# Performance work log

Hardware: AMD Instinct MI355X
Metric: run time of the kernel (lower is better)

Reference implementation:

```python
import jax, jax.numpy as jnp
import numpy as np

B, S, D, H, E, FF = 8, 512, 768, 12, 8, 3072
HD = D // H

def layernorm(x, g, b, eps=1e-5):
    mu = jnp.mean(x, axis=-1, keepdims=True)
    var = jnp.mean((x - mu) ** 2, axis=-1, keepdims=True)
    return (x - mu) * jax.lax.rsqrt(var + eps) * g + b

def setup_inputs() -> dict:
    key = jax.random.key(0)
    ks = jax.random.split(key, 16)
    sd = lambda n: 1.0 / np.sqrt(n)
    return {
        "x": jax.random.normal(ks[0], (B, S, D), jnp.float32),
        "indexes_list": jax.random.randint(ks[1], (1,), 0, E),
        "ln1_g": jnp.ones((D,), jnp.float32),
        "ln1_b": jnp.zeros((D,), jnp.float32),
        "qkv_w": jax.random.normal(ks[2], (D, 3 * D), jnp.float32) * sd(D),
        "proj_w": jax.random.normal(ks[3], (D, D), jnp.float32) * sd(D),
        "proj_b": jnp.zeros((D,), jnp.float32),
        "ln2_g": jnp.ones((D,), jnp.float32),
        "ln2_b": jnp.zeros((D,), jnp.float32),
        "switch_w": jax.random.normal(ks[4], (D, E), jnp.float32) * sd(D),
        "switch_b": jnp.zeros((E,), jnp.float32),
        "w1": jax.random.normal(ks[5], (E, D, FF), jnp.float32) * sd(D),
        "b1": jnp.zeros((E, FF), jnp.float32),
        "w2": jax.random.normal(ks[6], (E, FF, D), jnp.float32) * sd(FF),
        "b2": jnp.zeros((E, D), jnp.float32),
    }

def reference(x, indexes_list, ln1_g, ln1_b, qkv_w, proj_w, proj_b,
              ln2_g, ln2_b, switch_w, switch_b, w1, b1, w2, b2):
    # --- attention sublayer ---
    h = layernorm(x, ln1_g, ln1_b)
    qkv = (h @ qkv_w).reshape(B, S, 3, H, HD).transpose(2, 0, 3, 1, 4)  # [3,B,H,S,hd]
    q, k, v = qkv[0], qkv[1], qkv[2]
    scale = HD ** -0.5
    attn = jax.nn.softmax(jnp.einsum('bhqd,bhkd->bhqk', q, k) * scale, axis=-1)
    o = jnp.einsum('bhqk,bhkd->bhqd', attn, v).transpose(0, 2, 1, 3).reshape(B, S, D)
    x = x + o @ proj_w + proj_b
    # --- switch MoE sublayer (routes arg ignored, as in original) ---
    h = layernorm(x, ln2_g, ln2_b).reshape(B * S, D)  # [T,D]
    logits = h @ switch_w + switch_b
    routes = jnp.argmax(jax.nn.softmax(logits, axis=-1), axis=-1)  # [T]
    # dense per-expert compute, then select by route (same math as gather/scatter)
    y = jax.nn.gelu(jnp.einsum('td,edf->etf', h, w1) + b1[:, None, :], approximate=False)
    y = jax.nn.gelu(jnp.einsum('etf,efd->etd', y, w2) + b2[:, None, :], approximate=False)
    moe_out = y[routes, jnp.arange(B * S)]  # [T,D]
    return x + moe_out.reshape(B, S, D)
```

## Files before the change

### kernel.cpp

```cpp
#include <hip/hip_runtime.h>
#include <math.h>

#define T_TOK   4096
#define D_MODEL 768
#define H_HEADS 12
#define HDIM    64
#define S_SEQ   512
#define B_BATCH 8
#define E_EXP   8
#define FF_DIM  3072
#define MAX_TILES 40
#define MPAD_MAX  (MAX_TILES * 128)

typedef __attribute__((ext_vector_type(8))) short short8;
typedef __attribute__((ext_vector_type(4))) float floatx4;

__device__ __forceinline__ float gelu_exact(float x) {
    return 0.5f * x * (1.0f + erff(x * 0.7071067811865476f));
}

__device__ __forceinline__ unsigned short f2bf(float f) {
    unsigned int u = __float_as_uint(f);
    u += 0x7fffu + ((u >> 16) & 1u);
    return (unsigned short)(u >> 16);
}
__device__ __forceinline__ float bf2f(unsigned short h) {
    return __uint_as_float(((unsigned int)h) << 16);
}
__device__ __forceinline__ void split_bf(float v, unsigned short& hi, unsigned short& lo) {
    hi = f2bf(v);
    lo = f2bf(v - bf2f(hi));
}

__global__ void __launch_bounds__(256) ln_f32(const float* __restrict__ x,
                                              const float* __restrict__ g,
                                              const float* __restrict__ b,
                                              float* __restrict__ out) {
    int row = blockIdx.x;
    const float* xr = x + (size_t)row * D_MODEL;
    int tid = threadIdx.x;
    float v0 = xr[tid], v1 = xr[tid + 256], v2 = xr[tid + 512];
    float s = v0 + v1 + v2;
    float q = v0 * v0 + v1 * v1 + v2 * v2;
    for (int off = 32; off; off >>= 1) {
        s += __shfl_down(s, off);
        q += __shfl_down(q, off);
    }
    __shared__ float rs[4], rq[4], stats[2];
    int wid = tid >> 6, lane = tid & 63;
    if (lane == 0) { rs[wid] = s; rq[wid] = q; }
    __syncthreads();
    if (tid == 0) {
        float ts = rs[0] + rs[1] + rs[2] + rs[3];
        float tq = rq[0] + rq[1] + rq[2] + rq[3];
        float mu = ts * (1.0f / 768.0f);
        float var = tq * (1.0f / 768.0f) - mu * mu;
        stats[0] = mu; stats[1] = rsqrtf(var + 1e-5f);
    }
    __syncthreads();
    float mu = stats[0], rstd = stats[1];
    float* orow = out + (size_t)row * D_MODEL;
    orow[tid]       = (v0 - mu) * rstd * g[tid]       + b[tid];
    orow[tid + 256] = (v1 - mu) * rstd * g[tid + 256] + b[tid + 256];
    orow[tid + 512] = (v2 - mu) * rstd * g[tid + 512] + b[tid + 512];
}

__global__ void __launch_bounds__(256) ln_split(const float* __restrict__ x,
                                                const float* __restrict__ g,
                                                const float* __restrict__ b,
                                                unsigned short* __restrict__ ohi,
                                                unsigned short* __restrict__ olo) {
    int row = blockIdx.x;
    const float* xr = x + (size_t)row * D_MODEL;
    int tid = threadIdx.x;
    float v0 = xr[tid], v1 = xr[tid + 256], v2 = xr[tid + 512];
    float s = v0 + v1 + v2;
    float q = v0 * v0 + v1 * v1 + v2 * v2;
    for (int off = 32; off; off >>= 1) {
        s += __shfl_down(s, off);
        q += __shfl_down(q, off);
    }
    __shared__ float rs[4], rq[4], stats[2];
    int wid = tid >> 6, lane = tid & 63;
    if (lane == 0) { rs[wid] = s; rq[wid] = q; }
    __syncthreads();
    if (tid == 0) {
        float ts = rs[0] + rs[1] + rs[2] + rs[3];
        float tq = rq[0] + rq[1] + rq[2] + rq[3];
        float mu = ts * (1.0f / 768.0f);
        float var = tq * (1.0f / 768.0f) - mu * mu;
        stats[0] = mu; stats[1] = rsqrtf(var + 1e-5f);
    }
    __syncthreads();
    float mu = stats[0], rstd = stats[1];
    unsigned short* hr = ohi + (size_t)row * D_MODEL;
    unsigned short* lr = olo + (size_t)row * D_MODEL;
    float r0 = (v0 - mu) * rstd * g[tid]       + b[tid];
    float r1 = (v1 - mu) * rstd * g[tid + 256] + b[tid + 256];
    float r2 = (v2 - mu) * rstd * g[tid + 512] + b[tid + 512];
    unsigned short hi, lo;
    split_bf(r0, hi, lo); hr[tid] = hi;       lr[tid] = lo;
    split_bf(r1, hi, lo); hr[tid + 256] = hi; lr[tid + 256] = lo;
    split_bf(r2, hi, lo); hr[tid + 512] = hi; lr[tid + 512] = lo;
}

__global__ void __launch_bounds__(256) transpose_bf16(const float* __restrict__ in,
                                                      unsigned short* __restrict__ out,
                                                      int R, int C) {
    __shared__ float t[32][33];
    const float* inb = in + (size_t)blockIdx.z * R * C;
    unsigned short* outb = out + (size_t)blockIdx.z * R * C;
    int c0 = blockIdx.x * 32, r0 = blockIdx.y * 32;
    int tx = threadIdx.x & 31, ty = threadIdx.x >> 5;
#pragma unroll
    for (int rr = 0; rr < 32; rr += 8)
        t[ty + rr][tx] = inb[(size_t)(r0 + ty + rr) * C + c0 + tx];
    __syncthreads();
#pragma unroll
    for (int rr = 0; rr < 32; rr += 8)
        outb[(size_t)(c0 + ty + rr) * R + r0 + tx] = f2bf(t[tx][ty + rr]);
}

__global__ void __launch_bounds__(256) transpose_split(const float* __restrict__ in,
                                                       unsigned short* __restrict__ out_hi,
                                                       unsigned short* __restrict__ out_lo,
                                                       int R, int C) {
    __shared__ float t[32][33];
    int c0 = blockIdx.x * 32, r0 = blockIdx.y * 32;
    int tx = threadIdx.x & 31, ty = threadIdx.x >> 5;
#pragma unroll
    for (int rr = 0; rr < 32; rr += 8)
        t[ty + rr][tx] = in[(size_t)(r0 + ty + rr) * C + c0 + tx];
    __syncthreads();
#pragma unroll
    for (int rr = 0; rr < 32; rr += 8) {
        float v = t[tx][ty + rr];
        unsigned short hi, lo;
        split_bf(v, hi, lo);
        size_t idx = (size_t)(c0 + ty + rr) * R + r0 + tx;
        out_hi[idx] = hi;
        out_lo[idx] = lo;
    }
}

__global__ void __launch_bounds__(256) attn_tile(const float* __restrict__ qkv,
                                                 unsigned short* __restrict__ ohi,
                                                 unsigned short* __restrict__ olo) {
    __shared__ float Qst[64][68];
    __shared__ float Kst[64][68];
    __shared__ float Vs [64][68];
    int qt = blockIdx.x, hh = blockIdx.y, bb = blockIdx.z;
    int tid = threadIdx.x;
    int tx = tid & 15, ty = tid >> 4;
    const size_t rstride = 3 * D_MODEL;
    const float* base = qkv + (size_t)bb * S_SEQ * rstride + hh * HDIM;

    {
        int f4 = tid & 15;
        int r0 = tid >> 4;
        for (int rr = 0; rr < 64; rr += 16) {
            int r = r0 + rr;
            const float* qrow = base + (size_t)(qt * 64 + r) * rstride;
            float4 v = *(const float4*)(qrow + f4 * 4);
            Qst[f4 * 4 + 0][r] = v.x * 0.125f;
            Qst[f4 * 4 + 1][r] = v.y * 0.125f;
            Qst[f4 * 4 + 2][r] = v.z * 0.125f;
            Qst[f4 * 4 + 3][r] = v.w * 0.125f;
        }
    }

    float m_run[4], l_run[4], o_acc[4][4];
#pragma unroll
    for (int i = 0; i < 4; i++) {
        m_run[i] = -1e30f; l_run[i] = 0.f;
#pragma unroll
        for (int j2 = 0; j2 < 4; j2++) o_acc[i][j2] = 0.f;
    }

    for (int kt = 0; kt < 8; kt++) {
        __syncthreads();
        {
            int f4 = tid & 15;
            int r0 = tid >> 4;
            for (int rr = 0; rr < 64; rr += 16) {
                int r = r0 + rr;
                const float* krow = base + (size_t)(kt * 64 + r) * rstride + D_MODEL;
                float4 v = *(const float4*)(krow + f4 * 4);
                Kst[f4 * 4 + 0][r] = v.x;
                Kst[f4 * 4 + 1][r] = v.y;
                Kst[f4 * 4 + 2][r] = v.z;
                Kst[f4 * 4 + 3][r] = v.w;
                const float* vrow = base + (size_t)(kt * 64 + r) * rstride + 2 * D_MODEL;
                *(float4*)&Vs[r][f4 * 4] = *(const float4*)(vrow + f4 * 4);
            }
        }
        __syncthreads();

        float s[4][4] = {};
#pragma unroll 8
        for (int d = 0; d < 64; d++) {
            float4 a = *(const float4*)&Qst[d][ty * 4];
            float4 b = *(const float4*)&Kst[d][tx * 4];
            s[0][0] += a.x * b.x; s[0][1] += a.x * b.y; s[0][2] += a.x * b.z; s[0][3] += a.x * b.w;
            s[1][0] += a.y * b.x; s[1][1] += a.y * b.y; s[1][2] += a.y * b.z; s[1][3] += a.y * b.w;
            s[2][0] += a.z * b.x; s[2][1] += a.z * b.y; s[2][2] += a.z * b.z; s[2][3] += a.z * b.w;
            s[3][0] += a.w * b.x; s[3][1] += a.w * b.y; s[3][2] += a.w * b.z; s[3][3] += a.w * b.w;
        }
        __syncthreads();

#pragma unroll
        for (int i = 0; i < 4; i++) {
            float tm = fmaxf(fmaxf(s[i][0], s[i][1]), fmaxf(s[i][2], s[i][3]));
            tm = fmaxf(tm, __shfl_xor(tm, 1));
            tm = fmaxf(tm, __shfl_xor(tm, 2));
            tm = fmaxf(tm, __shfl_xor(tm, 4));
            tm = fmaxf(tm, __shfl_xor(tm, 8));
            float mn = fmaxf(m_run[i], tm);
            float alpha = __expf(m_run[i] - mn);
            m_run[i] = mn;
            float ts = 0.f;
#pragma unroll
            for (int j2 = 0; j2 < 4; j2++) {
                s[i][j2] = __expf(s[i][j2] - mn);
                ts += s[i][j2];
            }
            ts += __shfl_xor(ts, 1);
            ts += __shfl_xor(ts, 2);
            ts += __shfl_xor(ts, 4);
            ts += __shfl_xor(ts, 8);
            l_run[i] = l_run[i] * alpha + ts;
#pragma unroll
            for (int j2 = 0; j2 < 4; j2++) o_acc[i][j2] *= alpha;
        }

#pragma unroll
        for (int i = 0; i < 4; i++)
#pragma unroll
            for (int j2 = 0; j2 < 4; j2++)
                Kst[tx * 4 + j2][ty * 4 + i] = s[i][j2];
        __syncthreads();

#pragma unroll 8
        for (int k = 0; k < 64; k++) {
            float4 a = *(const float4*)&Kst[k][ty * 4];
            float4 b = *(const float4*)&Vs[k][tx * 4];
            o_acc[0][0] += a.x * b.x; o_acc[0][1] += a.x * b.y; o_acc[0][2] += a.x * b.z; o_acc[0][3] += a.x * b.w;
            o_acc[1][0] += a.y * b.x; o_acc[1][1] += a.y * b.y; o_acc[1][2] += a.y * b.z; o_acc[1][3] += a.y * b.w;
            o_acc[2][0] += a.z * b.x; o_acc[2][1] += a.z * b.y; o_acc[2][2] += a.z * b.z; o_acc[2][3] += a.z * b.w;
            o_acc[3][0] += a.w * b.x; o_acc[3][1] += a.w * b.y; o_acc[3][2] += a.w * b.z; o_acc[3][3] += a.w * b.w;
        }
    }

    size_t ob = (size_t)(bb * S_SEQ + qt * 64) * D_MODEL + hh * HDIM;
#pragma unroll
    for (int i = 0; i < 4; i++) {
        float inv = 1.0f / l_run[i];
        ushort4 rh, rl;
        unsigned short hi, lo;
        split_bf(o_acc[i][0] * inv, hi, lo); rh.x = hi; rl.x = lo;
        split_bf(o_acc[i][1] * inv, hi, lo); rh.y = hi; rl.y = lo;
        split_bf(o_acc[i][2] * inv, hi, lo); rh.z = hi; rl.z = lo;
        split_bf(o_acc[i][3] * inv, hi, lo); rh.w = hi; rl.w = lo;
        size_t idx = ob + (size_t)(ty * 4 + i) * D_MODEL + tx * 4;
        *(ushort4*)(ohi + idx) = rh;
        *(ushort4*)(olo + idx) = rl;
    }
}

__global__ void __launch_bounds__(64) router_kernel(const float* __restrict__ h2,
                                                    const float* __restrict__ sw,
                                                    const float* __restrict__ sb,
                                                    int* __restrict__ routes,
                                                    int* __restrict__ counts) {
    int t = blockIdx.x;
    int lane = threadIdx.x;
    const float* hr = h2 + (size_t)t * D_MODEL;
    float acc[8] = {};
    for (int d = lane; d < D_MODEL; d += 64) {
        float hv = hr[d];
        const float* wr = sw + (size_t)d * 8;
#pragma unroll
        for (int e = 0; e < 8; e++) acc[e] += hv * wr[e];
    }
#pragma unroll
    for (int e = 0; e < 8; e++)
        for (int off = 32; off; off >>= 1) acc[e] += __shfl_down(acc[e], off);
    if (lane == 0) {
        int best = 0;
        float bv = acc[0] + sb[0];
#pragma unroll
        for (int e = 1; e < 8; e++) {
            float v = acc[e] + sb[e];
            if (v > bv) { bv = v; best = e; }
        }
        routes[t] = best;
        atomicAdd(&counts[best], 1);
    }
}

__global__ void __launch_bounds__(256) init_kernel(int* counts, int* cursor, int* perm) {
    int idx = blockIdx.x * 256 + threadIdx.x;
    if (idx < MPAD_MAX) perm[idx] = -1;
    if (idx < 8) { counts[idx] = 0; cursor[idx] = 0; }
}

__global__ void moe_plan(const int* __restrict__ counts, int* pad_base,
                         int* tile_e, int* tile_row0, int* ntiles) {
    if (threadIdx.x == 0 && blockIdx.x == 0) {
        int base = 0, nt = 0;
        for (int e = 0; e < E_EXP; e++) {
            pad_base[e] = base;
            int c = counts[e];
            int nte = (c + 127) >> 7;
            for (int j = 0; j < nte; j++) {
                tile_e[nt] = e;
                tile_row0[nt] = base + j * 128;
                nt++;
            }
            base += nte * 128;
        }
        ntiles[0] = nt;
    }
}

__global__ void __launch_bounds__(256) scatter_kernel(const int* __restrict__ routes,
                                                      const int* __restrict__ pad_base,
                                                      int* __restrict__ cursor,
                                                      int* __restrict__ perm) {
    int t = blockIdx.x * 256 + threadIdx.x;
    if (t < T_TOK) {
        int e = routes[t];
        int pos = atomicAdd(&cursor[e], 1);
        perm[pad_base[e] + pos] = t;
    }
}

__global__ void __launch_bounds__(256) gather_bf16(const float* __restrict__ h2,
                                                   const int* __restrict__ perm,
                                                   unsigned short* __restrict__ Ag) {
    int g = blockIdx.x;
    int row = perm[g];
    unsigned short* dst = Ag + (size_t)g * D_MODEL;
    if (row >= 0) {
        const float* src = h2 + (size_t)row * D_MODEL;
        for (int d = threadIdx.x; d < D_MODEL; d += 256) dst[d] = f2bf(src[d]);
    } else {
        for (int d = threadIdx.x; d < D_MODEL; d += 256) dst[d] = 0;
    }
}

template <int MODE>
__global__ void __launch_bounds__(256) sgemm(const unsigned short* __restrict__ Ah_,
                                             const unsigned short* __restrict__ Al_,
                                             const unsigned short* __restrict__ Bh_,
                                             const unsigned short* __restrict__ Bl_,
                                             const float* __restrict__ bias,
                                             const float* __restrict__ resid,
                                             float* __restrict__ Cf,
                                             int N, int K) {
    __shared__ __align__(16) short Ah[128][40];
    __shared__ __align__(16) short Al[128][40];
    __shared__ __align__(16) short Bh[128][40];
    __shared__ __align__(16) short Bl[128][40];

    int row0 = blockIdx.y * 128, n0 = blockIdx.x * 128;
    int tid = threadIdx.x;
    int lane = tid & 63, wid = tid >> 6;
    int wr0 = (wid >> 1) * 64, wc0 = (wid & 1) * 64;
    int lm = lane & 15, q8 = (lane >> 4) * 8;
    int sr = tid >> 2;
    int sc = (tid & 3) * 8;

    floatx4 acc[4][4];
#pragma unroll
    for (int i = 0; i < 4; i++)
#pragma unroll
        for (int j = 0; j < 4; j++) acc[i][j] = (floatx4){0.f, 0.f, 0.f, 0.f};

    const unsigned short* Ahb = Ah_ + (size_t)row0 * K;
    const unsigned short* Alb = Al_ + (size_t)row0 * K;
    const unsigned short* Bhb = Bh_ + (size_t)n0 * K;
    const unsigned short* Blb = Bl_ + (size_t)n0 * K;

    for (int k0 = 0; k0 < K; k0 += 32) {
        *(uint4*)&Ah[sr][sc]      = *(const uint4*)(Ahb + (size_t)sr * K + k0 + sc);
        *(uint4*)&Ah[sr + 64][sc] = *(const uint4*)(Ahb + (size_t)(sr + 64) * K + k0 + sc);
        *(uint4*)&Al[sr][sc]      = *(const uint4*)(Alb + (size_t)sr * K + k0 + sc);
        *(uint4*)&Al[sr + 64][sc] = *(const uint4*)(Alb + (size_t)(sr + 64) * K + k0 + sc);
        *(uint4*)&Bh[sr][sc]      = *(const uint4*)(Bhb + (size_t)sr * K + k0 + sc);
        *(uint4*)&Bh[sr + 64][sc] = *(const uint4*)(Bhb + (size_t)(sr + 64) * K + k0 + sc);
        *(uint4*)&Bl[sr][sc]      = *(const uint4*)(Blb + (size_t)sr * K + k0 + sc);
        *(uint4*)&Bl[sr + 64][sc] = *(const uint4*)(Blb + (size_t)(sr + 64) * K + k0 + sc);
        __syncthreads();

        short8 ah[4], al[4], bh[4], bl[4];
#pragma unroll
        for (int i = 0; i < 4; i++) {
            ah[i] = *(const short8*)&Ah[wr0 + i * 16 + lm][q8];
            al[i] = *(const short8*)&Al[wr0 + i * 16 + lm][q8];
        }
#pragma unroll
        for (int j = 0; j < 4; j++) {
            bh[j] = *(const short8*)&Bh[wc0 + j * 16 + lm][q8];
            bl[j] = *(const short8*)&Bl[wc0 + j * 16 + lm][q8];
        }
#pragma unroll
        for (int i = 0; i < 4; i++)
#pragma unroll
            for (int j = 0; j < 4; j++) {
                acc[i][j] = __builtin_amdgcn_mfma_f32_16x16x32_bf16(ah[i], bh[j], acc[i][j], 0, 0, 0);
                acc[i][j] = __builtin_amdgcn_mfma_f32_16x16x32_bf16(ah[i], bl[j], acc[i][j], 0, 0, 0);
                acc[i][j] = __builtin_amdgcn_mfma_f32_16x16x32_bf16(al[i], bh[j], acc[i][j], 0, 0, 0);
            }
        __syncthreads();
    }

    int q4 = (lane >> 4) * 4;
#pragma unroll
    for (int i = 0; i < 4; i++) {
#pragma unroll
        for (int j = 0; j < 4; j++) {
            int c = n0 + wc0 + j * 16 + lm;
#pragma unroll
            for (int reg = 0; reg < 4; reg++) {
                int rloc = wr0 + i * 16 + q4 + reg;
                size_t idx = (size_t)(row0 + rloc) * N + c;
                float v = acc[i][j][reg];
                if constexpr (MODE == 0) Cf[idx] = v;
                else                     Cf[idx] = resid[idx] + v + bias[c];
            }
        }
    }
}

template <int MODE>
__global__ void __launch_bounds__(256) mgemm(const unsigned short* __restrict__ A,
                                             const unsigned short* __restrict__ Bt,
                                             const float* __restrict__ bias,
                                             const float* __restrict__ resid,
                                             float* __restrict__ Cf,
                                             unsigned short* __restrict__ Cb,
                                             int N, int K,
                                             const int* __restrict__ perm,
                                             const int* __restrict__ tile_e,
                                             const int* __restrict__ tile_row0,
                                             const int* __restrict__ ntiles) {
    __shared__ __align__(16) short As[128][40];
    __shared__ __align__(16) short Bs[128][40];

    if ((int)blockIdx.y >= ntiles[0]) return;
    int e = tile_e[blockIdx.y];
    int row0 = tile_row0[blockIdx.y];
    Bt += (size_t)e * N * K;
    bias += (size_t)e * N;
    int n0 = blockIdx.x * 128;

    int tid = threadIdx.x;
    int lane = tid & 63, wid = tid >> 6;
    int wr0 = (wid >> 1) * 64, wc0 = (wid & 1) * 64;
    int lm = lane & 15, q8 = (lane >> 4) * 8;
    int sr = tid >> 2;
    int sc = (tid & 3) * 8;

    floatx4 acc[4][4];
#pragma unroll
    for (int i = 0; i < 4; i++)
#pragma unroll
        for (int j = 0; j < 4; j++) acc[i][j] = (floatx4){0.f, 0.f, 0.f, 0.f};

    const unsigned short* Abase = A + (size_t)row0 * K;
    const unsigned short* Bbase = Bt + (size_t)n0 * K;

    for (int k0 = 0; k0 < K; k0 += 32) {
        *(uint4*)&As[sr][sc]      = *(const uint4*)(Abase + (size_t)sr * K + k0 + sc);
        *(uint4*)&As[sr + 64][sc] = *(const uint4*)(Abase + (size_t)(sr + 64) * K + k0 + sc);
        *(uint4*)&Bs[sr][sc]      = *(const uint4*)(Bbase + (size_t)sr * K + k0 + sc);
        *(uint4*)&Bs[sr + 64][sc] = *(const uint4*)(Bbase + (size_t)(sr + 64) * K + k0 + sc);
        __syncthreads();

        short8 af[4], bfr[4];
#pragma unroll
        for (int i = 0; i < 4; i++)
            af[i] = *(const short8*)&As[wr0 + i * 16 + lm][q8];
#pragma unroll
        for (int j = 0; j < 4; j++)
            bfr[j] = *(const short8*)&Bs[wc0 + j * 16 + lm][q8];
#pragma unroll
        for (int i = 0; i < 4; i++)
#pragma unroll
            for (int j = 0; j < 4; j++)
                acc[i][j] = __builtin_amdgcn_mfma_f32_16x16x32_bf16(af[i], bfr[j], acc[i][j], 0, 0, 0);
        __syncthreads();
    }

    int q4 = (lane >> 4) * 4;
#pragma unroll
    for (int i = 0; i < 4; i++) {
#pragma unroll
        for (int j = 0; j < 4; j++) {
            int c = n0 + wc0 + j * 16 + lm;
#pragma unroll
            for (int reg = 0; reg < 4; reg++) {
                int rloc = wr0 + i * 16 + q4 + reg;
                float v = acc[i][j][reg];
                if constexpr (MODE == 2) {
                    Cb[(size_t)(row0 + rloc) * N + c] = f2bf(gelu_exact(v + bias[c]));
                } else {
                    int t = perm[row0 + rloc];
                    if (t >= 0) {
                        size_t idx = (size_t)t * N + c;
                        Cf[idx] = resid[idx] + gelu_exact(v + bias[c]);
                    }
                }
            }
        }
    }
}

extern "C" void kernel_launch(void* const* d_in, const int* in_sizes, int n_in,
                              void* d_out, int out_size, void* d_ws, size_t ws_size,
                              hipStream_t stream) {
    const float* x      = (const float*)d_in[0];
    const float* ln1_g  = (const float*)d_in[2];
    const float* ln1_b  = (const float*)d_in[3];
    const float* qkv_w  = (const float*)d_in[4];
    const float* proj_w = (const float*)d_in[5];
    const float* proj_b = (const float*)d_in[6];
    const float* ln2_g  = (const float*)d_in[7];
    const float* ln2_b  = (const float*)d_in[8];
    const float* sw     = (const float*)d_in[9];
    const float* sb     = (const float*)d_in[10];
    const float* w1     = (const float*)d_in[11];
    const float* b1     = (const float*)d_in[12];
    const float* w2     = (const float*)d_in[13];
    const float* b2     = (const float*)d_in[14];
    float* out = (float*)d_out;

    char* p = (char*)d_ws;
    float*          qkv = (float*)p;
    float*          h   = (float*)p;
    unsigned short* y1  = (unsigned short*)p;
    p += (size_t)T_TOK * 2304 * 4;
    unsigned short* h_hi = (unsigned short*)p; p += (size_t)T_TOK * D_MODEL * 2;
    unsigned short* h_lo = (unsigned short*)p; p += (size_t)T_TOK * D_MODEL * 2;
    unsigned short* o_hi = h_hi;
    unsigned short* o_lo = h_lo;
    float* x1 = (float*)p; p += (size_t)T_TOK * D_MODEL * 4;
    unsigned short* Ag     = (unsigned short*)p;
    unsigned short* qwt_hi = (unsigned short*)p;
    unsigned short* qwt_lo = qwt_hi + (size_t)2304 * 768;
    p += (size_t)MPAD_MAX * D_MODEL * 2;
    unsigned short* pwt_hi = (unsigned short*)p; p += (size_t)768 * 768 * 2;
    unsigned short* pwt_lo = (unsigned short*)p; p += (size_t)768 * 768 * 2;
    unsigned short* w1t = (unsigned short*)p; p += (size_t)E_EXP * 3072 * 768 * 2;
    unsigned short* w2t = (unsigned short*)p; p += (size_t)E_EXP * 768 * 3072 * 2;
    int* routes    = (int*)p;
    int* perm      = routes + T_TOK;
    int* counts    = perm + MPAD_MAX;
    int* cursor    = counts + 8;
    int* pad_base  = cursor + 8;
    int* tile_e    = pad_base + 8;
    int* tile_row0 = tile_e + MAX_TILES;
    int* ntiles    = tile_row0 + MAX_TILES;

    transpose_split<<<dim3(2304 / 32, 768 / 32), 256, 0, stream>>>(qkv_w, qwt_hi, qwt_lo, 768, 2304);
    transpose_split<<<dim3(768 / 32, 768 / 32), 256, 0, stream>>>(proj_w, pwt_hi, pwt_lo, 768, 768);
    transpose_bf16<<<dim3(3072 / 32, 768 / 32, 8), 256, 0, stream>>>(w1, w1t, 768, 3072);
    transpose_bf16<<<dim3(768 / 32, 3072 / 32, 8), 256, 0, stream>>>(w2, w2t, 3072, 768);

    ln_split<<<T_TOK, 256, 0, stream>>>(x, ln1_g, ln1_b, h_hi, h_lo);
    sgemm<0><<<dim3(2304 / 128, T_TOK / 128), 256, 0, stream>>>(
        h_hi, h_lo, qwt_hi, qwt_lo, nullptr, nullptr, qkv, 2304, 768);
    attn_tile<<<dim3(S_SEQ / 64, H_HEADS, B_BATCH), 256, 0, stream>>>(qkv, o_hi, o_lo);
    sgemm<1><<<dim3(768 / 128, T_TOK / 128), 256, 0, stream>>>(
        o_hi, o_lo, pwt_hi, pwt_lo, proj_b, x, x1, 768, 768);
    ln_f32<<<T_TOK, 256, 0, stream>>>(x1, ln2_g, ln2_b, h);
    init_kernel<<<(MPAD_MAX + 255) / 256, 256, 0, stream>>>(counts, cursor, perm);
    router_kernel<<<T_TOK, 64, 0, stream>>>(h, sw, sb, routes, counts);
    moe_plan<<<1, 1, 0, stream>>>(counts, pad_base, tile_e, tile_row0, ntiles);
    scatter_kernel<<<T_TOK / 256, 256, 0, stream>>>(routes, pad_base, cursor, perm);
    gather_bf16<<<MPAD_MAX, 256, 0, stream>>>(h, perm, Ag);
    mgemm<2><<<dim3(FF_DIM / 128, MAX_TILES), 256, 0, stream>>>(
        Ag, w1t, b1, nullptr, nullptr, y1, FF_DIM, 768,
        perm, tile_e, tile_row0, ntiles);
    mgemm<3><<<dim3(D_MODEL / 128, MAX_TILES), 256, 0, stream>>>(
        y1, w2t, b2, x1, out, nullptr, D_MODEL, 3072,
        perm, tile_e, tile_row0, ntiles);
}
```

Before: 701.6 us.

## Rewrite attention kernel to use bf16x3 split MFMA instead of fp32 FMA

Replaces the scalar fp32 flash-attention tile kernel with one that computes QK^T and PV with 16x16x32 bf16 MFMA instructions. It keeps near-fp32 accuracy by splitting operands into hi/lo bf16 parts and issuing three MFMAs per product. K and V are converted to split bf16 in shared memory, and P is written back as split bf16 for the second matmul. This removes the large amount of fp32 FMA work in attention, at the cost of conversion overhead, strided transposed V stores to LDS, and scalar 2-byte output stores.

```diff
diff --git a/kernel.cpp b/kernel.cpp
--- a/kernel.cpp
+++ b/kernel.cpp
@@ -143,127 +143,161 @@
     }
 }
 
-__global__ void __launch_bounds__(256) attn_tile(const float* __restrict__ qkv,
+__global__ void __launch_bounds__(256) attn_mfma(const float* __restrict__ qkv,
                                                  unsigned short* __restrict__ ohi,
                                                  unsigned short* __restrict__ olo) {
-    __shared__ float Qst[64][68];
-    __shared__ float Kst[64][68];
-    __shared__ float Vs [64][68];
+    __shared__ __align__(16) short Kh[64][72], Kl[64][72];
+    __shared__ __align__(16) short Vh[64][72], Vl[64][72];
+
     int qt = blockIdx.x, hh = blockIdx.y, bb = blockIdx.z;
     int tid = threadIdx.x;
-    int tx = tid & 15, ty = tid >> 4;
+    int lane = tid & 63, wv = tid >> 6;
+    int lm = lane & 15, q8 = (lane >> 4) * 8, q4 = (lane >> 4) * 4;
     const size_t rstride = 3 * D_MODEL;
     const float* base = qkv + (size_t)bb * S_SEQ * rstride + hh * HDIM;
 
+    short8 qh[2], ql[2];
     {
-        int f4 = tid & 15;
-        int r0 = tid >> 4;
-        for (int rr = 0; rr < 64; rr += 16) {
-            int r = r0 + rr;
-            const float* qrow = base + (size_t)(qt * 64 + r) * rstride;
-            float4 v = *(const float4*)(qrow + f4 * 4);
-            Qst[f4 * 4 + 0][r] = v.x * 0.125f;
-            Qst[f4 * 4 + 1][r] = v.y * 0.125f;
-            Qst[f4 * 4 + 2][r] = v.z * 0.125f;
-            Qst[f4 * 4 + 3][r] = v.w * 0.125f;
-        }
-    }
-
-    float m_run[4], l_run[4], o_acc[4][4];
+        const float* qrow = base + (size_t)(qt * 64 + 16 * wv + lm) * rstride;
+#pragma unroll
+        for (int ks = 0; ks < 2; ks++) {
+            float4 v0 = *(const float4*)(qrow + ks * 32 + q8);
+            float4 v1 = *(const float4*)(qrow + ks * 32 + q8 + 4);
+            unsigned short h_, l_;
+            short8 sh, sl;
+            split_bf(v0.x * 0.125f, h_, l_); sh[0] = (short)h_; sl[0] = (short)l_;
+            split_bf(v0.y * 0.125f, h_, l_); sh[1] = (short)h_; sl[1] = (short)l_;
+            split_bf(v0.z * 0.125f, h_, l_); sh[2] = (short)h_; sl[2] = (short)l_;
+            split_bf(v0.w * 0.125f, h_, l_); sh[3] = (short)h_; sl[3] = (short)l_;
+            split_bf(v1.x * 0.125f, h_, l_); sh[4] = (short)h_; sl[4] = (short)l_;
+            split_bf(v1.y * 0.125f, h_, l_); sh[5] = (short)h_; sl[5] = (short)l_;
+            split_bf(v1.z * 0.125f, h_, l_); sh[6] = (short)h_; sl[6] = (short)l_;
+            split_bf(v1.w * 0.125f, h_, l_); sh[7] = (short)h_; sl[7] = (short)l_;
+            qh[ks] = sh; ql[ks] = sl;
+        }
+    }
+
+    float m_run[4], l_run[4];
+    floatx4 o_acc[4];
 #pragma unroll
     for (int i = 0; i < 4; i++) {
         m_run[i] = -1e30f; l_run[i] = 0.f;
-#pragma unroll
-        for (int j2 = 0; j2 < 4; j2++) o_acc[i][j2] = 0.f;
-    }
+        o_acc[i] = (floatx4){0.f, 0.f, 0.f, 0.f};
+    }
+
+    int sr = tid >> 2;
+    int sc0 = (tid & 3) * 16;
 
     for (int kt = 0; kt < 8; kt++) {
         __syncthreads();
         {
-            int f4 = tid & 15;
-            int r0 = tid >> 4;
-            for (int rr = 0; rr < 64; rr += 16) {
-                int r = r0 + rr;
-                const float* krow = base + (size_t)(kt * 64 + r) * rstride + D_MODEL;
-                float4 v = *(const float4*)(krow + f4 * 4);
-                Kst[f4 * 4 + 0][r] = v.x;
-                Kst[f4 * 4 + 1][r] = v.y;
-                Kst[f4 * 4 + 2][r] = v.z;
-                Kst[f4 * 4 + 3][r] = v.w;
-                const float* vrow = base + (size_t)(kt * 64 + r) * rstride + 2 * D_MODEL;
-                *(float4*)&Vs[r][f4 * 4] = *(const float4*)(vrow + f4 * 4);
-            }
-        }
-        __syncthreads();
-
-        float s[4][4] = {};
-#pragma unroll 8
-        for (int d = 0; d < 64; d++) {
-            float4 a = *(const float4*)&Qst[d][ty * 4];
-            float4 b = *(const float4*)&Kst[d][tx * 4];
-            s[0][0] += a.x * b.x; s[0][1] += a.x * b.y; s[0][2] += a.x * b.z; s[0][3] += a.x * b.w;
-            s[1][0] += a.y * b.x; s[1][1] += a.y * b.y; s[1][2] += a.y * b.z; s[1][3] += a.y * b.w;
-            s[2][0] += a.z * b.x; s[2][1] += a.z * b.y; s[2][2] += a.z * b.z; s[2][3] += a.z * b.w;
-            s[3][0] += a.w * b.x; s[3][1] += a.w * b.y; s[3][2] += a.w * b.z; s[3][3] += a.w * b.w;
-        }
-        __syncthreads();
-
-#pragma unroll
-        for (int i = 0; i < 4; i++) {
-            float tm = fmaxf(fmaxf(s[i][0], s[i][1]), fmaxf(s[i][2], s[i][3]));
+            const float* krow = base + (size_t)(kt * 64 + sr) * rstride + D_MODEL;
+            const float* vrow = krow + D_MODEL;
+#pragma unroll
+            for (int c = 0; c < 16; c += 4) {
+                float4 kv = *(const float4*)(krow + sc0 + c);
+                ushort4 h4, l4; unsigned short h_, l_;
+                split_bf(kv.x, h_, l_); h4.x = h_; l4.x = l_;
+                split_bf(kv.y, h_, l_); h4.y = h_; l4.y = l_;
+                split_bf(kv.z, h_, l_); h4.z = h_; l4.z = l_;
+                split_bf(kv.w, h_, l_); h4.w = h_; l4.w = l_;
+                *(ushort4*)&Kh[sr][sc0 + c] = h4;
+                *(ushort4*)&Kl[sr][sc0 + c] = l4;
+                float4 vv = *(const float4*)(vrow + sc0 + c);
+                split_bf(vv.x, h_, l_); Vh[sc0 + c + 0][sr] = (short)h_; Vl[sc0 + c + 0][sr] = (short)l_;
+                split_bf(vv.y, h_, l_); Vh[sc0 + c + 1][sr] = (short)h_; Vl[sc0 + c + 1][sr] = (short)l_;
+                split_bf(vv.z, h_, l_); Vh[sc0 + c + 2][sr] = (short)h_; Vl[sc0 + c + 2][sr] = (short)l_;
+                split_bf(vv.w, h_, l_); Vh[sc0 + c + 3][sr] = (short)h_; Vl[sc0 + c + 3][sr] = (short)l_;
+            }
+        }
+        __syncthreads();
+
+        floatx4 s_acc[4];
+#pragma unroll
+        for (int nt = 0; nt < 4; nt++) s_acc[nt] = (floatx4){0.f, 0.f, 0.f, 0.f};
+#pragma unroll
+        for (int ks = 0; ks < 2; ks++) {
+#pragma unroll
+            for (int nt = 0; nt < 4; nt++) {
+                short8 bh = *(const short8*)&Kh[nt * 16 + lm][ks * 32 + q8];
+                short8 bl = *(const short8*)&Kl[nt * 16 + lm][ks * 32 + q8];
+                s_acc[nt] = __builtin_amdgcn_mfma_f32_16x16x32_bf16(qh[ks], bh, s_acc[nt], 0, 0, 0);
+                s_acc[nt] = __builtin_amdgcn_mfma_f32_16x16x32_bf16(qh[ks], bl, s_acc[nt], 0, 0, 0);
+                s_acc[nt] = __builtin_amdgcn_mfma_f32_16x16x32_bf16(ql[ks], bh, s_acc[nt], 0, 0, 0);
+            }
+        }
+
+        float alpha_r[4];
+#pragma unroll
+        for (int reg = 0; reg < 4; reg++) {
+            float tm = fmaxf(fmaxf(s_acc[0][reg], s_acc[1][reg]),
+                             fmaxf(s_acc[2][reg], s_acc[3][reg]));
             tm = fmaxf(tm, __shfl_xor(tm, 1));
             tm = fmaxf(tm, __shfl_xor(tm, 2));
             tm = fmaxf(tm, __shfl_xor(tm, 4));
             tm = fmaxf(tm, __shfl_xor(tm, 8));
-            float mn = fmaxf(m_run[i], tm);
-            float alpha = __expf(m_run[i] - mn);
-            m_run[i] = mn;
+            float mn = fmaxf(m_run[reg], tm);
+            alpha_r[reg] = __expf(m_run[reg] - mn);
+            m_run[reg] = mn;
             float ts = 0.f;
 #pragma unroll
-            for (int j2 = 0; j2 < 4; j2++) {
-                s[i][j2] = __expf(s[i][j2] - mn);
-                ts += s[i][j2];
+            for (int nt = 0; nt < 4; nt++) {
+                float pv = __expf(s_acc[nt][reg] - mn);
+                s_acc[nt][reg] = pv;
+                ts += pv;
             }
             ts += __shfl_xor(ts, 1);
             ts += __shfl_xor(ts, 2);
             ts += __shfl_xor(ts, 4);
             ts += __shfl_xor(ts, 8);
-            l_run[i] = l_run[i] * alpha + ts;
-#pragma unroll
-            for (int j2 = 0; j2 < 4; j2++) o_acc[i][j2] *= alpha;
-        }
-
-#pragma unroll
-        for (int i = 0; i < 4; i++)
-#pragma unroll
-            for (int j2 = 0; j2 < 4; j2++)
-                Kst[tx * 4 + j2][ty * 4 + i] = s[i][j2];
-        __syncthreads();
-
-#pragma unroll 8
-        for (int k = 0; k < 64; k++) {
-            float4 a = *(const float4*)&Kst[k][ty * 4];
-            float4 b = *(const float4*)&Vs[k][tx * 4];
-            o_acc[0][0] += a.x * b.x; o_acc[0][1] += a.x * b.y; o_acc[0][2] += a.x * b.z; o_acc[0][3] += a.x * b.w;
-            o_acc[1][0] += a.y * b.x; o_acc[1][1] += a.y * b.y; o_acc[1][2] += a.y * b.z; o_acc[1][3] += a.y * b.w;
-            o_acc[2][0] += a.z * b.x; o_acc[2][1] += a.z * b.y; o_acc[2][2] += a.z * b.z; o_acc[2][3] += a.z * b.w;
-            o_acc[3][0] += a.w * b.x; o_acc[3][1] += a.w * b.y; o_acc[3][2] += a.w * b.z; o_acc[3][3] += a.w * b.w;
+            l_run[reg] = l_run[reg] * alpha_r[reg] + ts;
+        }
+
+        __syncthreads();
+
+#pragma unroll
+        for (int nt = 0; nt < 4; nt++)
+#pragma unroll
+            for (int reg = 0; reg < 4; reg++) {
+                unsigned short h_, l_;
+                split_bf(s_acc[nt][reg], h_, l_);
+                Kh[16 * wv + q4 + reg][nt * 16 + lm] = (short)h_;
+                Kl[16 * wv + q4 + reg][nt * 16 + lm] = (short)l_;
+            }
+#pragma unroll
+        for (int nt = 0; nt < 4; nt++)
+#pragma unroll
+            for (int reg = 0; reg < 4; reg++) o_acc[nt][reg] *= alpha_r[reg];
+
+        __syncthreads();
+
+#pragma unroll
+        for (int ks = 0; ks < 2; ks++) {
+            short8 ph = *(const short8*)&Kh[16 * wv + lm][ks * 32 + q8];
+            short8 pl = *(const short8*)&Kl[16 * wv + lm][ks * 32 + q8];
+#pragma unroll
+            for (int nt = 0; nt < 4; nt++) {
+                short8 vh = *(const short8*)&Vh[nt * 16 + lm][ks * 32 + q8];
+                short8 vl = *(const short8*)&Vl[nt * 16 + lm][ks * 32 + q8];
+                o_acc[nt] = __builtin_amdgcn_mfma_f32_16x16x32_bf16(ph, vh, o_acc[nt], 0, 0, 0);
+                o_acc[nt] = __builtin_amdgcn_mfma_f32_16x16x32_bf16(ph, vl, o_acc[nt], 0, 0, 0);
+                o_acc[nt] = __builtin_amdgcn_mfma_f32_16x16x32_bf16(pl, vh, o_acc[nt], 0, 0, 0);
+            }
         }
     }
 
     size_t ob = (size_t)(bb * S_SEQ + qt * 64) * D_MODEL + hh * HDIM;
 #pragma unroll
-    for (int i = 0; i < 4; i++) {
-        float inv = 1.0f / l_run[i];
-        ushort4 rh, rl;
-        unsigned short hi, lo;
-        split_bf(o_acc[i][0] * inv, hi, lo); rh.x = hi; rl.x = lo;
-        split_bf(o_acc[i][1] * inv, hi, lo); rh.y = hi; rl.y = lo;
-        split_bf(o_acc[i][2] * inv, hi, lo); rh.z = hi; rl.z = lo;
-        split_bf(o_acc[i][3] * inv, hi, lo); rh.w = hi; rl.w = lo;
-        size_t idx = ob + (size_t)(ty * 4 + i) * D_MODEL + tx * 4;
-        *(ushort4*)(ohi + idx) = rh;
-        *(ushort4*)(olo + idx) = rl;
+    for (int reg = 0; reg < 4; reg++) {
+        float inv = 1.0f / l_run[reg];
+#pragma unroll
+        for (int nt = 0; nt < 4; nt++) {
+            unsigned short h_, l_;
+            split_bf(o_acc[nt][reg] * inv, h_, l_);
+            size_t idx = ob + (size_t)(16 * wv + q4 + reg) * D_MODEL + nt * 16 + lm;
+            ohi[idx] = h_;
+            olo[idx] = l_;
+        }
     }
 }
 
@@ -571,7 +605,7 @@
     ln_split<<<T_TOK, 256, 0, stream>>>(x, ln1_g, ln1_b, h_hi, h_lo);
     sgemm<0><<<dim3(2304 / 128, T_TOK / 128), 256, 0, stream>>>(
         h_hi, h_lo, qwt_hi, qwt_lo, nullptr, nullptr, qkv, 2304, 768);
-    attn_tile<<<dim3(S_SEQ / 64, H_HEADS, B_BATCH), 256, 0, stream>>>(qkv, o_hi, o_lo);
+    attn_mfma<<<dim3(S_SEQ / 64, H_HEADS, B_BATCH), 256, 0, stream>>>(qkv, o_hi, o_lo);
     sgemm<1><<<dim3(768 / 128, T_TOK / 128), 256, 0, stream>>>(
         o_hi, o_lo, pwt_hi, pwt_lo, proj_b, x, x1, 768, 768);
     ln_f32<<<T_TOK, 256, 0, stream>>>(x1, ln2_g, ln2_b, h);
```

Result: faster. 650.9 us (-7.2%).
